# Performance work log

Measured on AMD Instinct MI355X. Metric: run time of the kernel, lower is better.

Reference implementation:

```python
import jax, jax.numpy as jnp
import numpy as np

INPUT_SIZE = 256
OUTPUT_SIZE = 128
N = 8192
SLOPE = 0.01
NEG_BIG = -9e15


def setup_inputs() -> dict:
    key = jax.random.key(0)
    k_h, k_adj, k_W, k_a = jax.random.split(key, 4)
    h = jax.random.normal(k_h, (N, INPUT_SIZE), dtype=jnp.float32)
    adj = jax.random.randint(k_adj, (N, N), 0, 2, dtype=jnp.int32)
    # xavier_uniform with gain=1.414
    gain = 1.414
    lim_W = gain * np.sqrt(6.0 / (INPUT_SIZE + OUTPUT_SIZE))
    W = jax.random.uniform(k_W, (INPUT_SIZE, OUTPUT_SIZE), dtype=jnp.float32, minval=-lim_W, maxval=lim_W)
    lim_a = gain * np.sqrt(6.0 / (2 * OUTPUT_SIZE + 1))
    a = jax.random.uniform(k_a, (2 * OUTPUT_SIZE, 1), dtype=jnp.float32, minval=-lim_a, maxval=lim_a)
    return {"h": h, "adj": adj, "W": W, "a": a}


def reference(h, adj, W, a):
    # Wh: [N, F]
    Wh = h @ W
    Fo = Wh.shape[1]
    # Original builds [N, N, 2F] concat then matmul with a; equivalent to
    # e[i, j] = leaky_relu(Wh[i] . a[:F] + Wh[j] . a[F:]) via broadcasting.
    src = Wh @ a[:Fo, 0]   # [N]
    dst = Wh @ a[Fo:, 0]   # [N]
    e = jax.nn.leaky_relu(src[:, None] + dst[None, :], negative_slope=SLOPE)  # [N, N]
    att = jnp.where(adj > 0, e, NEG_BIG)
    att = jax.nn.softmax(att, axis=1)
    return att @ Wh
```

## Files before the change

kernel.cpp:

```cpp
#include <hip/hip_runtime.h>
#include <hip/hip_bf16.h>

typedef unsigned short u16;
typedef unsigned int u32;
typedef __attribute__((ext_vector_type(8))) short short8;
typedef __attribute__((ext_vector_type(4))) float f32x4;

#define NN 8192
#define KIN 256
#define FOUT 128
#define SPLITS 8
#define KPER (NN / SPLITS)
#define KSTEPS (KPER / 32)
#define L2E 1.4426950408889634f

__device__ __forceinline__ float exp2fast(float x) { return __builtin_amdgcn_exp2f(x); }

__device__ __forceinline__ u16 f2bf(float f) {
    u32 u = __float_as_uint(f);
    u32 r = ((u >> 16) & 1u) + 0x7fffu;
    return (u16)((u + r) >> 16);
}
__device__ __forceinline__ u32 pk_bf16(float a, float b) {
    union { __hip_bfloat162 h2; u32 u; } cv;
    cv.h2 = __float22bfloat162_rn(make_float2(a, b));
    return cv.u;
}
__device__ __forceinline__ u32 fkey(float f) {
    u32 b = __float_as_uint(f);
    return (b & 0x80000000u) ? ~b : (b | 0x80000000u);
}
__device__ __forceinline__ float funkey(u32 k) {
    u32 b = (k & 0x80000000u) ? (k & 0x7fffffffu) : ~k;
    return __uint_as_float(b);
}

__global__ __launch_bounds__(256) void k1_wh(
    const float* __restrict__ h, const float* __restrict__ W, const float* __restrict__ a,
    u16* __restrict__ whfrag,
    float* __restrict__ src, float* __restrict__ dl2e, u32* __restrict__ gmaxk)
{
    __shared__ float hT[64][36];
    __shared__ u16   lt[128][40];
    __shared__ float sd[32][2];
    const int t  = threadIdx.x;
    const int m0 = blockIdx.x * 32;
    const int rq = t >> 5, cq = t & 31;

    float acc[4][4];
#pragma unroll
    for (int i = 0; i < 4; i++)
#pragma unroll
        for (int j = 0; j < 4; j++) acc[i][j] = 0.f;
    if (t < 64) sd[t >> 1][t & 1] = 0.f;

    for (int kt = 0; kt < KIN; kt += 64) {
        __syncthreads();
#pragma unroll
        for (int s2 = 0; s2 < 2; s2++) {
            int f = s2 * 256 + t;
            int r = f >> 4, kc = (f & 15) * 4;
            float4 hv = *(const float4*)(h + (size_t)(m0 + r) * KIN + kt + kc);
            hT[kc + 0][r] = hv.x; hT[kc + 1][r] = hv.y;
            hT[kc + 2][r] = hv.z; hT[kc + 3][r] = hv.w;
        }
        __syncthreads();
        for (int k = 0; k < 64; k++) {
            float4 wv = *(const float4*)(W + (size_t)(kt + k) * FOUT + cq * 4);
            float h0 = hT[k][rq * 4 + 0], h1 = hT[k][rq * 4 + 1];
            float h2 = hT[k][rq * 4 + 2], h3 = hT[k][rq * 4 + 3];
            acc[0][0] += h0 * wv.x; acc[0][1] += h0 * wv.y; acc[0][2] += h0 * wv.z; acc[0][3] += h0 * wv.w;
            acc[1][0] += h1 * wv.x; acc[1][1] += h1 * wv.y; acc[1][2] += h1 * wv.z; acc[1][3] += h1 * wv.w;
            acc[2][0] += h2 * wv.x; acc[2][1] += h2 * wv.y; acc[2][2] += h2 * wv.z; acc[2][3] += h2 * wv.w;
            acc[3][0] += h3 * wv.x; acc[3][1] += h3 * wv.y; acc[3][2] += h3 * wv.z; acc[3][3] += h3 * wv.w;
        }
    }
#pragma unroll
    for (int i = 0; i < 4; i++) {
        float sp = 0.f, dp = 0.f;
#pragma unroll
        for (int j = 0; j < 4; j++) {
            sp += acc[i][j] * a[cq * 4 + j];
            dp += acc[i][j] * a[FOUT + cq * 4 + j];
            lt[cq * 4 + j][rq * 4 + i] = f2bf(acc[i][j]);
        }
        atomicAdd(&sd[rq * 4 + i][0], sp);
        atomicAdd(&sd[rq * 4 + i][1], dp);
    }
    __syncthreads();
    if (t < 32) { src[m0 + t] = sd[t][0]; dl2e[m0 + t] = sd[t][1] * L2E; }
    if (t < 64) {
        float v = (t < 32) ? sd[t][1] : -3.0e38f;
#pragma unroll
        for (int off = 32; off >= 1; off >>= 1) v = fmaxf(v, __shfl_down(v, off));
        if (t == 0) atomicMax(gmaxk, fkey(v));
    }
    const int kstep = blockIdx.x;
#pragma unroll
    for (int p = 0; p < 2; p++) {
        int f = p * 256 + t;
        int nt = f >> 6;
        int l  = f & 63;
        short8 v = *(const short8*)&lt[nt * 16 + (l & 15)][(l >> 4) * 8];
        *(short8*)(whfrag + ((size_t)(kstep * 8 + nt) * 64 + l) * 8) = v;
    }
}

__global__ __launch_bounds__(256, 4) void k2_attn(
    const int* __restrict__ adj, const float* __restrict__ src, const float* __restrict__ dl2e,
    const u16* __restrict__ whfrag, const u32* __restrict__ gmaxk,
    float* __restrict__ accp, float* __restrict__ lp)
{
    const int t = threadIdx.x;
    const int lane = t & 63, wave = t >> 6;
    const int strip = blockIdx.x * 4 + wave;
    const int i0 = strip * 16;
    const int split = blockIdx.y;
    const int l15 = lane & 15;
    const int kq = (lane >> 4) * 8;

    float sp = src[i0 + l15] * L2E;
    float gm = funkey(*gmaxk) * L2E;
    float xx = sp + gm;
    float C = fmaxf(xx, 0.01f * xx);
    const float y1 = sp - C, y2 = 0.01f * sp - C;

    const int* arow = adj + (size_t)(i0 + l15) * NN;
    const int st0 = blockIdx.x & (KSTEPS - 1);
    const int kbase = split * KPER;

    f32x4 acc[8];
#pragma unroll
    for (int nt = 0; nt < 8; nt++) acc[nt] = {0.f, 0.f, 0.f, 0.f};
    float psum = 0.f;

    int4 aL[2], aH[2]; float4 dL[2], dH[2];
#pragma unroll
    for (int s = 0; s < 2; s++) {
        int kb = kbase + ((st0 + s) & (KSTEPS - 1)) * 32;
        aL[s] = *(const int4*)(arow + kb + kq);
        aH[s] = *(const int4*)(arow + kb + kq + 4);
        dL[s] = *(const float4*)(dl2e + kb + kq);
        dH[s] = *(const float4*)(dl2e + kb + kq + 4);
    }

#pragma unroll 4
    for (int it = 0; it < KSTEPS; ++it) {
        const int sl = it & 1;
        const int kb = kbase + ((st0 + it) & (KSTEPS - 1)) * 32;

        uint4 bv[8];
        const u16* wf = whfrag + ((size_t)(kb >> 5) * 8 * 64 + lane) * 8;
#pragma unroll
        for (int nt = 0; nt < 8; nt++)
            bv[nt] = *(const uint4*)(wf + (size_t)nt * 64 * 8);

        int4 al = aL[sl], ah = aH[sl];
        float4 dl = dL[sl], dh = dH[sl];
        float p0, p1, p2, p3, p4, p5, p6, p7;
        {
            float x;
            x = fmaxf(y1 + dl.x, y2 + 0.01f * dl.x); p0 = exp2fast(al.x > 0 ? x : -1.0e9f);
            x = fmaxf(y1 + dl.y, y2 + 0.01f * dl.y); p1 = exp2fast(al.y > 0 ? x : -1.0e9f);
            x = fmaxf(y1 + dl.z, y2 + 0.01f * dl.z); p2 = exp2fast(al.z > 0 ? x : -1.0e9f);
            x = fmaxf(y1 + dl.w, y2 + 0.01f * dl.w); p3 = exp2fast(al.w > 0 ? x : -1.0e9f);
            x = fmaxf(y1 + dh.x, y2 + 0.01f * dh.x); p4 = exp2fast(ah.x > 0 ? x : -1.0e9f);
            x = fmaxf(y1 + dh.y, y2 + 0.01f * dh.y); p5 = exp2fast(ah.y > 0 ? x : -1.0e9f);
            x = fmaxf(y1 + dh.z, y2 + 0.01f * dh.z); p6 = exp2fast(ah.z > 0 ? x : -1.0e9f);
            x = fmaxf(y1 + dh.w, y2 + 0.01f * dh.w); p7 = exp2fast(ah.w > 0 ? x : -1.0e9f);
        }
        psum += ((p0 + p1) + (p2 + p3)) + ((p4 + p5) + (p6 + p7));
        union { short8 s8; u32 u[4]; } af;
        af.u[0] = pk_bf16(p0, p1); af.u[1] = pk_bf16(p2, p3);
        af.u[2] = pk_bf16(p4, p5); af.u[3] = pk_bf16(p6, p7);

        {
            int kb2 = kbase + ((st0 + it + 2) & (KSTEPS - 1)) * 32;
            aL[sl] = *(const int4*)(arow + kb2 + kq);
            aH[sl] = *(const int4*)(arow + kb2 + kq + 4);
            dL[sl] = *(const float4*)(dl2e + kb2 + kq);
            dH[sl] = *(const float4*)(dl2e + kb2 + kq + 4);
        }

#pragma unroll
        for (int nt = 0; nt < 8; nt++) {
            union { uint4 q; short8 s8; } bf; bf.q = bv[nt];
            acc[nt] = __builtin_amdgcn_mfma_f32_16x16x32_bf16(af.s8, bf.s8, acc[nt], 0, 0, 0);
        }
    }

    float v = psum;
    v += __shfl_down(v, 32);
    v += __shfl_down(v, 16);
    if (lane < 16) lp[split * NN + i0 + lane] = v;

    float* ab = accp + (size_t)split * (NN * FOUT);
#pragma unroll
    for (int nt = 0; nt < 8; nt++)
        *(f32x4*)&ab[((size_t)(strip * 8 + nt) * 64 + lane) * 4] = acc[nt];
}

__global__ __launch_bounds__(256) void k2b_rsum(const float* __restrict__ lp,
                                               float* __restrict__ rinv)
{
    int i = blockIdx.x * 256 + threadIdx.x;
    float s = 0.f;
#pragma unroll
    for (int sp = 0; sp < SPLITS; sp++) s += lp[sp * NN + i];
    rinv[i] = 1.0f / s;
}

__global__ __launch_bounds__(256) void k3_comb(
    const float* __restrict__ accp, const float* __restrict__ rinv, float* __restrict__ out)
{
    int idx = blockIdx.x * 256 + threadIdx.x;
    int tile = idx >> 6, l = idx & 63;
    float4 s = make_float4(0.f, 0.f, 0.f, 0.f);
#pragma unroll
    for (int sp = 0; sp < SPLITS; sp++) {
        float4 v = *(const float4*)(accp + (size_t)sp * (NN * FOUT) + (size_t)idx * 4);
        s.x += v.x; s.y += v.y; s.z += v.z; s.w += v.w;
    }
    int row0 = (tile >> 3) * 16 + (l >> 4) * 4;
    int col  = (tile & 7) * 16 + (l & 15);
    float4 ri = *(const float4*)(rinv + row0);
    out[(size_t)(row0 + 0) * FOUT + col] = s.x * ri.x;
    out[(size_t)(row0 + 1) * FOUT + col] = s.y * ri.y;
    out[(size_t)(row0 + 2) * FOUT + col] = s.z * ri.z;
    out[(size_t)(row0 + 3) * FOUT + col] = s.w * ri.w;
}

extern "C" void kernel_launch(void* const* d_in, const int* in_sizes, int n_in,
                              void* d_out, int out_size, void* d_ws, size_t ws_size,
                              hipStream_t stream) {
    const float* h   = (const float*)d_in[0];
    const int*   adj = (const int*)d_in[1];
    const float* W   = (const float*)d_in[2];
    const float* a   = (const float*)d_in[3];
    float* out = (float*)d_out;

    char* ws = (char*)d_ws;
    u16*   whfrag = (u16*)ws;
    float* src    = (float*)(ws + (2u << 20));
    float* dl2e   = src + NN;
    u32*   gmaxk  = (u32*)(dl2e + NN);
    float* accp   = (float*)(ws + (3u << 20));
    float* lp     = (float*)(ws + (35u << 20));
    float* rinv   = (float*)(ws + (36u << 20));

    (void)hipMemsetAsync(gmaxk, 0, sizeof(u32), stream);
    k1_wh<<<dim3(NN / 32), dim3(256), 0, stream>>>(h, W, a, whfrag, src, dl2e, gmaxk);
    k2_attn<<<dim3(NN / 64, SPLITS), dim3(256), 0, stream>>>(adj, src, dl2e, whfrag, gmaxk, accp, lp);
    k2b_rsum<<<dim3(NN / 256), dim3(256), 0, stream>>>(lp, rinv);
    k3_comb<<<dim3((NN * FOUT / 4) / 256), dim3(256), 0, stream>>>(accp, rinv, out);
}
```

Before: 447.4 us.

## Pack adjacency into bitmask in a pre-pass and read bits in attention kernel

```diff
diff --git a/kernel.cpp b/kernel.cpp
--- a/kernel.cpp
+++ b/kernel.cpp
@@ -3,6 +3,7 @@
 
 typedef unsigned short u16;
 typedef unsigned int u32;
+typedef unsigned long long u64;
 typedef __attribute__((ext_vector_type(8))) short short8;
 typedef __attribute__((ext_vector_type(4))) float f32x4;
 
@@ -12,6 +13,7 @@
 #define SPLITS 8
 #define KPER (NN / SPLITS)
 #define KSTEPS (KPER / 32)
+#define NWORDS (NN / 32)
 #define L2E 1.4426950408889634f
 
 __device__ __forceinline__ float exp2fast(float x) { return __builtin_amdgcn_exp2f(x); }
@@ -33,6 +35,20 @@
 __device__ __forceinline__ float funkey(u32 k) {
     u32 b = (k & 0x80000000u) ? (k & 0x7fffffffu) : ~k;
     return __uint_as_float(b);
+}
+
+__global__ __launch_bounds__(256) void k0_pack(const int* __restrict__ adj,
+                                               u64* __restrict__ bm)
+{
+    const int lane = threadIdx.x & 63;
+    const u32 wid = (blockIdx.x * 256 + threadIdx.x) >> 6;
+    const u32 nw  = (gridDim.x * 256) >> 6;
+    const u32 total = (u32)(((size_t)NN * NN) >> 6);
+    for (u32 c = wid; c < total; c += nw) {
+        int v = adj[(size_t)c * 64 + lane];
+        u64 b = __ballot(v > 0);
+        if (lane == 0) bm[c] = b;
+    }
 }
 
 __global__ __launch_bounds__(256) void k1_wh(
@@ -107,7 +123,7 @@
 }
 
 __global__ __launch_bounds__(256, 4) void k2_attn(
-    const int* __restrict__ adj, const float* __restrict__ src, const float* __restrict__ dl2e,
+    const u32* __restrict__ bmask, const float* __restrict__ src, const float* __restrict__ dl2e,
     const u16* __restrict__ whfrag, const u32* __restrict__ gmaxk,
     float* __restrict__ accp, float* __restrict__ lp)
 {
@@ -125,7 +141,7 @@
     float C = fmaxf(xx, 0.01f * xx);
     const float y1 = sp - C, y2 = 0.01f * sp - C;
 
-    const int* arow = adj + (size_t)(i0 + l15) * NN;
+    const u32* brow = bmask + (size_t)(i0 + l15) * NWORDS;
     const int st0 = blockIdx.x & (KSTEPS - 1);
     const int kbase = split * KPER;
 
@@ -134,19 +150,8 @@
     for (int nt = 0; nt < 8; nt++) acc[nt] = {0.f, 0.f, 0.f, 0.f};
     float psum = 0.f;
 
-    int4 aL[2], aH[2]; float4 dL[2], dH[2];
-#pragma unroll
-    for (int s = 0; s < 2; s++) {
-        int kb = kbase + ((st0 + s) & (KSTEPS - 1)) * 32;
-        aL[s] = *(const int4*)(arow + kb + kq);
-        aH[s] = *(const int4*)(arow + kb + kq + 4);
-        dL[s] = *(const float4*)(dl2e + kb + kq);
-        dH[s] = *(const float4*)(dl2e + kb + kq + 4);
-    }
-
 #pragma unroll 4
     for (int it = 0; it < KSTEPS; ++it) {
-        const int sl = it & 1;
         const int kb = kbase + ((st0 + it) & (KSTEPS - 1)) * 32;
 
         uint4 bv[8];
@@ -155,33 +160,27 @@
         for (int nt = 0; nt < 8; nt++)
             bv[nt] = *(const uint4*)(wf + (size_t)nt * 64 * 8);
 
-        int4 al = aL[sl], ah = aH[sl];
-        float4 dl = dL[sl], dh = dH[sl];
+        const u32 ab = brow[kb >> 5] >> kq;
+        const float4 dl = *(const float4*)(dl2e + kb + kq);
+        const float4 dh = *(const float4*)(dl2e + kb + kq + 4);
+
         float p0, p1, p2, p3, p4, p5, p6, p7;
         {
             float x;
-            x = fmaxf(y1 + dl.x, y2 + 0.01f * dl.x); p0 = exp2fast(al.x > 0 ? x : -1.0e9f);
-            x = fmaxf(y1 + dl.y, y2 + 0.01f * dl.y); p1 = exp2fast(al.y > 0 ? x : -1.0e9f);
-            x = fmaxf(y1 + dl.z, y2 + 0.01f * dl.z); p2 = exp2fast(al.z > 0 ? x : -1.0e9f);
-            x = fmaxf(y1 + dl.w, y2 + 0.01f * dl.w); p3 = exp2fast(al.w > 0 ? x : -1.0e9f);
-            x = fmaxf(y1 + dh.x, y2 + 0.01f * dh.x); p4 = exp2fast(ah.x > 0 ? x : -1.0e9f);
-            x = fmaxf(y1 + dh.y, y2 + 0.01f * dh.y); p5 = exp2fast(ah.y > 0 ? x : -1.0e9f);
-            x = fmaxf(y1 + dh.z, y2 + 0.01f * dh.z); p6 = exp2fast(ah.z > 0 ? x : -1.0e9f);
-            x = fmaxf(y1 + dh.w, y2 + 0.01f * dh.w); p7 = exp2fast(ah.w > 0 ? x : -1.0e9f);
+            x = fmaxf(y1 + dl.x, y2 + 0.01f * dl.x); p0 = exp2fast((ab &   1u) ? x : -1.0e9f);
+            x = fmaxf(y1 + dl.y, y2 + 0.01f * dl.y); p1 = exp2fast((ab &   2u) ? x : -1.0e9f);
+            x = fmaxf(y1 + dl.z, y2 + 0.01f * dl.z); p2 = exp2fast((ab &   4u) ? x : -1.0e9f);
+            x = fmaxf(y1 + dl.w, y2 + 0.01f * dl.w); p3 = exp2fast((ab &   8u) ? x : -1.0e9f);
+            x = fmaxf(y1 + dh.x, y2 + 0.01f * dh.x); p4 = exp2fast((ab &  16u) ? x : -1.0e9f);
+            x = fmaxf(y1 + dh.y, y2 + 0.01f * dh.y); p5 = exp2fast((ab &  32u) ? x : -1.0e9f);
+            x = fmaxf(y1 + dh.z, y2 + 0.01f * dh.z); p6 = exp2fast((ab &  64u) ? x : -1.0e9f);
+            x = fmaxf(y1 + dh.w, y2 + 0.01f * dh.w); p7 = exp2fast((ab & 128u) ? x : -1.0e9f);
         }
         psum += ((p0 + p1) + (p2 + p3)) + ((p4 + p5) + (p6 + p7));
         union { short8 s8; u32 u[4]; } af;
         af.u[0] = pk_bf16(p0, p1); af.u[1] = pk_bf16(p2, p3);
         af.u[2] = pk_bf16(p4, p5); af.u[3] = pk_bf16(p6, p7);
 
-        {
-            int kb2 = kbase + ((st0 + it + 2) & (KSTEPS - 1)) * 32;
-            aL[sl] = *(const int4*)(arow + kb2 + kq);
-            aH[sl] = *(const int4*)(arow + kb2 + kq + 4);
-            dL[sl] = *(const float4*)(dl2e + kb2 + kq);
-            dH[sl] = *(const float4*)(dl2e + kb2 + kq + 4);
-        }
-
 #pragma unroll
         for (int nt = 0; nt < 8; nt++) {
             union { uint4 q; short8 s8; } bf; bf.q = bv[nt];
@@ -194,10 +193,10 @@
     v += __shfl_down(v, 16);
     if (lane < 16) lp[split * NN + i0 + lane] = v;
 
-    float* ab = accp + (size_t)split * (NN * FOUT);
+    float* ab2 = accp + (size_t)split * (NN * FOUT);
 #pragma unroll
     for (int nt = 0; nt < 8; nt++)
-        *(f32x4*)&ab[((size_t)(strip * 8 + nt) * 64 + lane) * 4] = acc[nt];
+        *(f32x4*)&ab2[((size_t)(strip * 8 + nt) * 64 + lane) * 4] = acc[nt];
 }
 
 __global__ __launch_bounds__(256) void k2b_rsum(const float* __restrict__ lp,
@@ -247,10 +246,12 @@
     float* accp   = (float*)(ws + (3u << 20));
     float* lp     = (float*)(ws + (35u << 20));
     float* rinv   = (float*)(ws + (36u << 20));
+    u64*   bmask  = (u64*)(ws + (37u << 20));
 
     (void)hipMemsetAsync(gmaxk, 0, sizeof(u32), stream);
+    k0_pack<<<dim3(2048), dim3(256), 0, stream>>>(adj, bmask);
     k1_wh<<<dim3(NN / 32), dim3(256), 0, stream>>>(h, W, a, whfrag, src, dl2e, gmaxk);
-    k2_attn<<<dim3(NN / 64, SPLITS), dim3(256), 0, stream>>>(adj, src, dl2e, whfrag, gmaxk, accp, lp);
+    k2_attn<<<dim3(NN / 64, SPLITS), dim3(256), 0, stream>>>((const u32*)bmask, src, dl2e, whfrag, gmaxk, accp, lp);
     k2b_rsum<<<dim3(NN / 256), dim3(256), 0, stream>>>(lp, rinv);
     k3_comb<<<dim3((NN * FOUT / 4) / 256), dim3(256), 0, stream>>>(accp, rinv, out);
 }
```

Result: slower. 489.1 us (+9.3%).
